# Optimization experiments

Hardware: AMD Instinct MI355X
Metric: run time of the kernel (lower is better)

The kernel has to match this reference:

```python
import jax, jax.numpy as jnp
import numpy as np

B, DIM, N = 4, 256, 2048
DIM_CTX, M = 256, 2048
HEADS, DIM_HEAD = 8, 64
DIM_INNER = HEADS * DIM_HEAD  # 512
EPS = 1e-12  # matches F.normalize eps


def setup_inputs() -> dict:
    key = jax.random.key(0)
    ks = jax.random.split(key, 8)
    return {
        "fmap": jax.random.normal(ks[0], (B, DIM, N), dtype=jnp.float32),
        "context": jax.random.normal(ks[1], (B, DIM_CTX, M), dtype=jnp.float32),
        "mask": jax.random.randint(ks[2], (B, M), 0, 2) > 0,
        "gamma": jnp.ones((DIM, 1), dtype=jnp.float32),
        "gamma_ctx": jnp.ones((DIM_CTX, 1), dtype=jnp.float32),
        "Wq": jax.random.normal(ks[3], (DIM_INNER, DIM), dtype=jnp.float32) * (DIM ** -0.5),
        "Wkv": jax.random.normal(ks[4], (2 * DIM_INNER, DIM_CTX), dtype=jnp.float32) * (DIM_CTX ** -0.5),
        "Wout": jax.random.normal(ks[5], (DIM, DIM_INNER), dtype=jnp.float32) * (DIM_INNER ** -0.5),
    }


def channel_rmsnorm(x, gamma):
    # F.normalize(x, dim=1) * sqrt(dim) * gamma ; x: [b, c, n], gamma: [c, 1]
    scale = x.shape[1] ** 0.5
    norm = jnp.sqrt(jnp.sum(x * x, axis=1, keepdims=True))
    normed = x / jnp.maximum(norm, EPS)
    return normed * scale * gamma[None]


def reference(fmap, context, mask, gamma, gamma_ctx, Wq, Wkv, Wout):
    h, d = HEADS, DIM_HEAD
    attn_scale = d ** -0.5

    fmap_n = channel_rmsnorm(fmap, gamma)          # [b, dim, n]
    ctx_n = channel_rmsnorm(context, gamma_ctx)    # [b, dim_ctx, m]

    # 1x1 Conv1d == matmul over channels
    q = jnp.einsum('oc,bcn->bon', Wq, fmap_n)      # [b, h*d, n]
    kv = jnp.einsum('oc,bcm->bom', Wkv, ctx_n)     # [b, 2*h*d, m]
    k, v = jnp.split(kv, 2, axis=1)

    # [b, h*d, n] -> [b, h, n, d]
    def to_heads(t):
        b, _, nn = t.shape
        return t.reshape(b, h, d, nn).transpose(0, 1, 3, 2)

    q, k, v = to_heads(q), to_heads(k), to_heads(v)

    # L2-distance attention: sim = -||q_i - k_j||_2 * scale
    q2 = jnp.sum(q * q, axis=-1)                   # [b, h, n]
    k2 = jnp.sum(k * k, axis=-1)                   # [b, h, m]
    qk = jnp.einsum('bhid,bhjd->bhij', q, k)       # [b, h, n, m]
    d2 = jnp.maximum(q2[..., :, None] + k2[..., None, :] - 2.0 * qk, 0.0)
    dist = jnp.sqrt(jnp.maximum(d2, EPS))
    sim = -dist * attn_scale

    neg_max = -jnp.finfo(sim.dtype).max
    sim = jnp.where(mask[:, None, None, :], sim, neg_max)

    attn = jax.nn.softmax(sim, axis=-1)            # [b, h, n, m]
    out = jnp.einsum('bhij,bhjd->bhid', attn, v)   # [b, h, n, d]
    out = out.transpose(0, 1, 3, 2).reshape(out.shape[0], h * d, -1)  # [b, h*d, n]
    return jnp.einsum('oc,bcn->bon', Wout, out)    # [b, dim, n]
```

## Files before the change

### kernel.cpp

```cpp
#include <hip/hip_runtime.h>
#include <hip/hip_bf16.h>

#define B_ 4
#define DIM_ 256
#define N_ 2048
#define M_ 2048
#define HEADS_ 8
#define DHEAD_ 64
#define DINNER_ 512

typedef __attribute__((ext_vector_type(8))) short short8;
typedef __attribute__((ext_vector_type(4))) short short4v;
typedef __attribute__((ext_vector_type(4))) float floatx4;
typedef __attribute__((ext_vector_type(4))) _Float16 half4;
typedef __attribute__((ext_vector_type(8))) _Float16 half8;

#if defined(__has_builtin)
#if __has_builtin(__builtin_amdgcn_global_load_lds)
#define HAS_DMA 1
#endif
#endif

typedef __attribute__((address_space(1))) const void gvoid_t;
typedef __attribute__((address_space(3))) void lvoid_t;

__device__ inline short bf16r(float x) {
  unsigned u = __float_as_uint(x);
  unsigned r = (u + 0x7fffu + ((u >> 16) & 1u)) >> 16;
  return (short)r;
}
__device__ inline float bf2f(short b) {
  return __uint_as_float(((unsigned)(unsigned short)b) << 16);
}

__global__ __launch_bounds__(256) void wsplit_kernel(
    const float* __restrict__ Wq, const float* __restrict__ Wkv,
    const float* __restrict__ Wout, const float* __restrict__ gamma,
    const float* __restrict__ gctx, short* __restrict__ whi,
    short* __restrict__ wlo) {
  const int y = blockIdx.y;
  const int gsz[3] = {32768, 65536, 32768};
  const int goff[3] = {0, 131072, 393216};
  int gidx = blockIdx.x * 256 + threadIdx.x;
  if (gidx >= gsz[y]) return;
  const float* W = (y == 0) ? Wq : (y == 1) ? Wkv : Wout;
  const int cmask = (y == 2) ? 511 : 255;
  int e0 = gidx * 4;
  int c = e0 & cmask;
  float4 wv = *(const float4*)&W[e0];
  if (y < 2) {
    const float* g = (y == 0) ? gamma : gctx;
    float4 g4 = *(const float4*)&g[c];
    wv.x *= g4.x; wv.y *= g4.y; wv.z *= g4.z; wv.w *= g4.w;
  }
  float vv[4] = {wv.x, wv.y, wv.z, wv.w};
  short4v hi, lo;
#pragma unroll
  for (int e = 0; e < 4; ++e) {
    short hb = bf16r(vv[e]);
    hi[e] = hb;
    lo[e] = bf16r(vv[e] - bf2f(hb));
  }
  *(short4v*)&whi[goff[y] + e0] = hi;
  *(short4v*)&wlo[goff[y] + e0] = lo;
}

__global__ __launch_bounds__(256) void colnorm_t_kernel(
    const float* __restrict__ xf, const float* __restrict__ xc,
    short* __restrict__ xtf, short* __restrict__ xtc, int NN) {
  const float* x = (blockIdx.z == 0) ? xf : xc;
  short* xt = (blockIdx.z == 0) ? xtf : xtc;
  int b = blockIdx.y;
  int tx = threadIdx.x, ty = threadIdx.y;
  int n0 = blockIdx.x * 64, n = n0 + tx;
  const float* xb = x + (size_t)b * 256 * NN;

  float ssq = 0.f;
  for (int c = ty; c < 256; c += 4) {
    float v = xb[(size_t)c * NN + n];
    ssq += v * v;
  }
  __shared__ float red[4][64];
  __shared__ float scl[64];
  __shared__ float t[64][65];
  red[ty][tx] = ssq;
  __syncthreads();
  if (ty == 0) {
    float s = red[0][tx] + red[1][tx] + red[2][tx] + red[3][tx];
    scl[tx] = 16.0f / fmaxf(sqrtf(s), 1e-12f);
  }
  int tid = ty * 64 + tx;
  int row = tid >> 2, cg = tid & 3;
  for (int c0 = 0; c0 < 256; c0 += 64) {
    __syncthreads();
    for (int cc = ty; cc < 64; cc += 4) t[cc][tx] = xb[(size_t)(c0 + cc) * NN + n];
    __syncthreads();
    float sc = scl[row];
    short8 o0v, o1v;
#pragma unroll
    for (int e = 0; e < 8; ++e) {
      o0v[e] = bf16r(t[cg * 16 + e][row] * sc);
      o1v[e] = bf16r(t[cg * 16 + 8 + e][row] * sc);
    }
    size_t base = ((size_t)b * NN + n0 + row) * 256 + c0 + cg * 16;
    *(short8*)&xt[base] = o0v;
    *(short8*)&xt[base + 8] = o1v;
  }
}

__global__ __launch_bounds__(256) void qkv_gemm_kernel(
    const short* __restrict__ whi, const short* __restrict__ wlo,
    const short* __restrict__ fmap_t, const short* __restrict__ ctx_t,
    short* __restrict__ qb, short* __restrict__ kc, _Float16* __restrict__ vc,
    const int* __restrict__ maskp, float* __restrict__ k2m) {
  const int b = blockIdx.z;
  const int y = blockIdx.y;
  const bool isq = (y < 4);
  const int o0 = (isq ? y : y - 4) * 128;
  const int n0 = blockIdx.x * 128;
  const short* Wh = whi + (isq ? 0 : 131072);
  const short* Wl = wlo + (isq ? 0 : 131072);
  const short* Xt = isq ? fmap_t : ctx_t;

  const int tid = threadIdx.x;
  const int w = tid >> 6, l = tid & 63, quad = l >> 4, l15 = l & 15;
  const int wo = (w >> 1) * 64, wn = (w & 1) * 64;

  __shared__ __align__(16) short Wa[2][128][40];
  __shared__ __align__(16) short Xb[128][40];

  floatx4 acc[4][4];
#pragma unroll
  for (int ot = 0; ot < 4; ++ot)
#pragma unroll
    for (int nt = 0; nt < 4; ++nt)
#pragma unroll
      for (int r = 0; r < 4; ++r) acc[ot][nt][r] = 0.f;

  for (int c0 = 0; c0 < 256; c0 += 32) {
    __syncthreads();
#pragma unroll
    for (int it = 0; it < 2; ++it) {
      int lin = tid + it * 256;
      int row = lin >> 2, sg = (lin & 3) * 8;
      size_t src = (size_t)(o0 + row) * 256 + c0 + sg;
      *(short8*)&Wa[0][row][sg] = *(const short8*)&Wh[src];
      *(short8*)&Wa[1][row][sg] = *(const short8*)&Wl[src];
    }
#pragma unroll
    for (int it = 0; it < 2; ++it) {
      int lin = tid + it * 256;
      int nn = lin >> 2, sg = (lin & 3) * 8;
      *(short8*)&Xb[nn][sg] =
          *(const short8*)&Xt[((size_t)b * 2048 + n0 + nn) * 256 + c0 + sg];
    }
    __syncthreads();

    short8 ah[4], al[4], bx[4];
#pragma unroll
    for (int ot = 0; ot < 4; ++ot) {
      ah[ot] = *(const short8*)&Wa[0][wo + 16 * ot + l15][8 * quad];
      al[ot] = *(const short8*)&Wa[1][wo + 16 * ot + l15][8 * quad];
    }
#pragma unroll
    for (int nt = 0; nt < 4; ++nt)
      bx[nt] = *(const short8*)&Xb[wn + 16 * nt + l15][8 * quad];
#pragma unroll
    for (int ot = 0; ot < 4; ++ot)
#pragma unroll
      for (int nt = 0; nt < 4; ++nt) {
        acc[ot][nt] =
            __builtin_amdgcn_mfma_f32_16x16x32_bf16(al[ot], bx[nt], acc[ot][nt], 0, 0, 0);
        acc[ot][nt] =
            __builtin_amdgcn_mfma_f32_16x16x32_bf16(ah[ot], bx[nt], acc[ot][nt], 0, 0, 0);
      }
  }

  if (isq) {
#pragma unroll
    for (int nt = 0; nt < 4; ++nt) {
      int n = n0 + wn + 16 * nt + l15;
      size_t base = ((size_t)b * 2048 + n) * 512;
#pragma unroll
      for (int ot = 0; ot < 4; ++ot) {
        int o = o0 + wo + 16 * ot + 4 * quad;
        short4v pk;
#pragma unroll
        for (int r = 0; r < 4; ++r) pk[r] = bf16r(acc[ot][nt][r]);
        *(short4v*)&qb[base + o] = pk;
      }
    }
  } else if (o0 < 512) {
    const int head = (o0 + wo) >> 6;
    const int bh = b * 8 + head;
    float k2p[4] = {0.f, 0.f, 0.f, 0.f};
#pragma unroll
    for (int nt = 0; nt < 4; ++nt) {
      int m = n0 + wn + 16 * nt + l15;
      int chunk = m >> 6, mrow = m & 63;
      size_t tbase = (((size_t)bh * 32 + chunk) * 64 + mrow) * 64;
      int sw = mrow & 7;
#pragma unroll
      for (int ot = 0; ot < 4; ++ot) {
        int d0 = 16 * ot + 4 * quad;
        short4v pk;
#pragma unroll
        for (int r = 0; r < 4; ++r) {
          short pv = bf16r(-2.0f * acc[ot][nt][r]);
          pk[r] = pv;
          float kr = bf2f(pv);
          k2p[nt] += kr * kr;
        }
        *(short4v*)&kc[tbase + (size_t)(((d0 >> 3) ^ sw) << 3) + (d0 & 7)] = pk;
      }
    }
#pragma unroll
    for (int nt = 0; nt < 4; ++nt) {
      float s = k2p[nt];
      s += __shfl_xor(s, 16);
      s += __shfl_xor(s, 32);
      if (quad == 0) {
        int m = n0 + wn + 16 * nt + l15;
        int mv = maskp[b * 2048 + m];
        k2m[(size_t)bh * 2048 + m] = mv ? 0.25f * s : __builtin_inff();
      }
    }
  } else {
    const int chv = o0 - 512 + wo;
    const int bh = b * 8 + (chv >> 6);
#pragma unroll
    for (int nt = 0; nt < 4; ++nt) {
      int j = n0 + wn + 16 * nt + l15;
      int chunk = j >> 6, jr = j & 63;
      int jrem = jr & 31;
      int colp = 32 * (jr >> 5) + ((jrem >> 2) & 3) * 8 + (jrem >> 4) * 4 +
                 (jrem & 3);
      size_t cbase = ((size_t)bh * 32 + chunk) * 4096;
#pragma unroll
      for (int ot = 0; ot < 4; ++ot)
#pragma unroll
        for (int r = 0; r < 4; ++r) {
          int drow = (chv + 16 * ot + 4 * quad + r) & 63;
          vc[cbase + drow * 64 + (((colp >> 3) ^ (drow & 7)) << 3) +
             (colp & 7)] = (_Float16)acc[ot][nt][r];
        }
    }
  }
}

__global__ __launch_bounds__(256, 4) void attn_kernel(
    const short* __restrict__ qb, const short* __restrict__ kc,
    const _Float16* __restrict__ vc, const float* __restrict__ k2m,
    short* __restrict__ attn_t) {
  const int bid = blockIdx.x;
  const int rr = bid & 7, qq = bid >> 3;
  const int bh = rr * 4 + (qq >> 5);
  const int iblk = qq & 31;
  const int h = bh & 7, b = bh >> 3;
  const int i0 = iblk * 64;

  const int tid = threadIdx.x;
  const int w = tid >> 6, l = tid & 63, quad = l >> 4, l15 = l & 15;

  __shared__ __align__(16) short kbuf[2][4096];
  __shared__ __align__(16) short vbuf[2][4096];

  const short* qrow =
      qb + ((size_t)b * 2048 + i0 + 16 * w + l15) * 512 + h * 64;
  const short* kcb = kc + (size_t)bh * 32 * 4096;
  const _Float16* vcb = vc + (size_t)bh * 32 * 4096;
  const float* k2b = k2m + (size_t)bh * 2048;

  short8 qa0 = *(const short8*)&qrow[8 * quad];
  short8 qa1 = *(const short8*)&qrow[32 + 8 * quad];
  float q2p = 0.f;
#pragma unroll
  for (int jj = 0; jj < 8; ++jj) {
    float f0 = bf2f(qa0[jj]), f1 = bf2f(qa1[jj]);
    q2p += f0 * f0 + f1 * f1;
  }
  q2p += __shfl_xor(q2p, 16);
  q2p += __shfl_xor(q2p, 32);
  const float q2c = q2p;

  floatx4 accO[4];
#pragma unroll
  for (int dt = 0; dt < 4; ++dt)
#pragma unroll
    for (int r = 0; r < 4; ++r) accO[dt][r] = 0.f;
  float lsum = 0.f;

  const float C2 = -0.18033688011112042f;
  const int sx = l15 & 7;

  auto stage = [&](int c, int p) {
    const short* ks = kcb + (size_t)c * 4096 + (2 * w) * 512 + l * 8;
    const _Float16* vs = vcb + (size_t)c * 4096 + (2 * w) * 512 + l * 8;
#ifdef HAS_DMA
    __builtin_amdgcn_global_load_lds((gvoid_t*)ks,
                                     (lvoid_t*)&kbuf[p][(2 * w) * 512], 16, 0, 0);
    __builtin_amdgcn_global_load_lds((gvoid_t*)(ks + 512),
                                     (lvoid_t*)&kbuf[p][(2 * w + 1) * 512], 16, 0, 0);
    __builtin_amdgcn_global_load_lds((gvoid_t*)vs,
                                     (lvoid_t*)&vbuf[p][(2 * w) * 512], 16, 0, 0);
    __builtin_amdgcn_global_load_lds((gvoid_t*)(vs + 512),
                                     (lvoid_t*)&vbuf[p][(2 * w + 1) * 512], 16, 0, 0);
#else
    *(short8*)&kbuf[p][(2 * w) * 512 + l * 8] = *(const short8*)ks;
    *(short8*)&kbuf[p][(2 * w + 1) * 512 + l * 8] = *(const short8*)(ks + 512);
    *(half8*)&vbuf[p][(2 * w) * 512 + l * 8] = *(const half8*)vs;
    *(half8*)&vbuf[p][(2 * w + 1) * 512 + l * 8] = *(const half8*)(vs + 512);
#endif
  };

  float4 k2pref[4];
#pragma unroll
  for (int jt = 0; jt < 4; ++jt)
    k2pref[jt] = *(const float4*)&k2b[16 * jt + 4 * quad];

  stage(0, 0);
  for (int c = 0; c < 32; ++c) {
    __syncthreads();
    if (c < 31) stage(c + 1, (c + 1) & 1);
    const int p = c & 1;

    float4 k2cur[4];
#pragma unroll
    for (int jt = 0; jt < 4; ++jt) k2cur[jt] = k2pref[jt];
    if (c < 31) {
#pragma unroll
      for (int jt = 0; jt < 4; ++jt)
        k2pref[jt] = *(const float4*)&k2b[(c + 1) * 64 + 16 * jt + 4 * quad];
    }

    half4 pb[4];
#pragma unroll
    for (int jt = 0; jt < 4; ++jt) {
      const short* kr = &kbuf[p][(16 * jt + l15) * 64];
      short8 k0 = *(const short8*)&kr[(quad ^ sx) << 3];
      short8 k1 = *(const short8*)&kr[((quad + 4) ^ sx) << 3];
      floatx4 a;
      a[0] = q2c; a[1] = q2c; a[2] = q2c; a[3] = q2c;
      a = __builtin_amdgcn_mfma_f32_16x16x32_bf16(k0, qa0, a, 0, 0, 0);
      a = __builtin_amdgcn_mfma_f32_16x16x32_bf16(k1, qa1, a, 0, 0, 0);
      float k2a[4] = {k2cur[jt].x, k2cur[jt].y, k2cur[jt].z, k2cur[jt].w};
#pragma unroll
      for (int r = 0; r < 4; ++r) {
        float d2 = fmaxf(a[r] + k2a[r], 1e-12f);
        float pv = __builtin_amdgcn_exp2f(C2 * __builtin_amdgcn_sqrtf(d2));
        lsum += pv;
        pb[jt][r] = (_Float16)pv;
      }
    }

#pragma unroll
    for (int dt = 0; dt < 4; ++dt) {
      const _Float16* vr = (const _Float16*)&vbuf[p][(16 * dt + l15) * 64];
      half8 h0 = *(const half8*)&vr[(quad ^ sx) << 3];
      half8 h1 = *(const half8*)&vr[((quad + 4) ^ sx) << 3];
      half4 va00 = __builtin_shufflevector(h0, h0, 0, 1, 2, 3);
      half4 va01 = __builtin_shufflevector(h0, h0, 4, 5, 6, 7);
      half4 va10 = __builtin_shufflevector(h1, h1, 0, 1, 2, 3);
      half4 va11 = __builtin_shufflevector(h1, h1, 4, 5, 6, 7);
      accO[dt] = __builtin_amdgcn_mfma_f32_16x16x16f16(va00, pb[0], accO[dt], 0, 0, 0);
      accO[dt] = __builtin_amdgcn_mfma_f32_16x16x16f16(va01, pb[1], accO[dt], 0, 0, 0);
      accO[dt] = __builtin_amdgcn_mfma_f32_16x16x16f16(va10, pb[2], accO[dt], 0, 0, 0);
      accO[dt] = __builtin_amdgcn_mfma_f32_16x16x16f16(va11, pb[3], accO[dt], 0, 0, 0);
    }
  }

  lsum += __shfl_xor(lsum, 16);
  lsum += __shfl_xor(lsum, 32);
  float rl = 1.0f / lsum;
  size_t base = ((size_t)b * 2048 + i0 + 16 * w + l15) * 512 + h * 64;
#pragma unroll
  for (int dt = 0; dt < 4; ++dt)
#pragma unroll
    for (int r = 0; r < 4; ++r)
      attn_t[base + 16 * dt + 4 * quad + r] = bf16r(accO[dt][r] * rl);
}

__global__ __launch_bounds__(256) void outproj_kernel(
    const short* __restrict__ whi, const short* __restrict__ wlo,
    const short* __restrict__ Xt, float* __restrict__ Yf) {
  const int b = blockIdx.z;
  const int n0 = blockIdx.x * 128;
  const int o0 = blockIdx.y * 64;
  const int tid = threadIdx.x;
  const int w = tid >> 6, l = tid & 63, quad = l >> 4, l15 = l & 15;
  const int wo = (w >> 1) * 32, wn = (w & 1) * 64;

  __shared__ __align__(16) short Wa[2][64][40];
  __shared__ __align__(16) short Xb[128][40];

  floatx4 acc[2][4];
#pragma unroll
  for (int ot = 0; ot < 2; ++ot)
#pragma unroll
    for (int nt = 0; nt < 4; ++nt)
#pragma unroll
      for (int r = 0; r < 4; ++r) acc[ot][nt][r] = 0.f;

  for (int c0 = 0; c0 < 512; c0 += 32) {
    __syncthreads();
    {
      int row = tid >> 2, sg = (tid & 3) * 8;
      size_t src = (size_t)(o0 + row) * 512 + c0 + sg;
      *(short8*)&Wa[0][row][sg] = *(const short8*)&whi[src];
      *(short8*)&Wa[1][row][sg] = *(const short8*)&wlo[src];
    }
#pragma unroll
    for (int it = 0; it < 2; ++it) {
      int lin = tid + it * 256;
      int nn = lin >> 2, sg = (lin & 3) * 8;
      *(short8*)&Xb[nn][sg] =
          *(const short8*)&Xt[((size_t)b * 2048 + n0 + nn) * 512 + c0 + sg];
    }
    __syncthreads();

    short8 ah[2], al[2], bx[4];
#pragma unroll
    for (int ot = 0; ot < 2; ++ot) {
      ah[ot] = *(const short8*)&Wa[0][wo + 16 * ot + l15][8 * quad];
      al[ot] = *(const short8*)&Wa[1][wo + 16 * ot + l15][8 * quad];
    }
#pragma unroll
    for (int nt = 0; nt < 4; ++nt)
      bx[nt] = *(const short8*)&Xb[wn + 16 * nt + l15][8 * quad];
#pragma unroll
    for (int ot = 0; ot < 2; ++ot)
#pragma unroll
      for (int nt = 0; nt < 4; ++nt) {
        acc[ot][nt] =
            __builtin_amdgcn_mfma_f32_16x16x32_bf16(al[ot], bx[nt], acc[ot][nt], 0, 0, 0);
        acc[ot][nt] =
            __builtin_amdgcn_mfma_f32_16x16x32_bf16(ah[ot], bx[nt], acc[ot][nt], 0, 0, 0);
      }
  }

#pragma unroll
  for (int ot = 0; ot < 2; ++ot)
#pragma unroll
    for (int r = 0; r < 4; ++r) {
      int o = o0 + wo + 16 * ot + 4 * quad + r;
#pragma unroll
      for (int nt = 0; nt < 4; ++nt)
        Yf[((size_t)b * 256 + o) * 2048 + n0 + wn + 16 * nt + l15] =
            acc[ot][nt][r];
    }
}

extern "C" void kernel_launch(void* const* d_in, const int* in_sizes, int n_in,
                              void* d_out, int out_size, void* d_ws,
                              size_t ws_size, hipStream_t stream) {
  const float* fmap = (const float*)d_in[0];
  const float* context = (const float*)d_in[1];
  const int* mask = (const int*)d_in[2];
  const float* gamma = (const float*)d_in[3];
  const float* gamma_ctx = (const float*)d_in[4];
  const float* Wq = (const float*)d_in[5];
  const float* Wkv = (const float*)d_in[6];
  const float* Wout = (const float*)d_in[7];
  float* out = (float*)d_out;

  char* ws = (char*)d_ws;
  short* fmap_t = (short*)ws;
  short* ctx_t = fmap_t + 2097152;
  short* qb = ctx_t + 2097152;
  short* kc = qb + 4194304;
  _Float16* vc = (_Float16*)(kc + 4194304);
  short* attn_t = (short*)(vc + 4194304);
  float* k2m = (float*)(attn_t + 4194304);
  short* whi = (short*)(k2m + 65536);
  short* wlo = whi + 524288;

  dim3 blk64x4(64, 4);
  wsplit_kernel<<<dim3(256, 3), 256, 0, stream>>>(Wq, Wkv, Wout, gamma,
                                                  gamma_ctx, whi, wlo);
  colnorm_t_kernel<<<dim3(32, B_, 2), blk64x4, 0, stream>>>(
      fmap, context, fmap_t, ctx_t, N_);
  qkv_gemm_kernel<<<dim3(16, 12, B_), 256, 0, stream>>>(
      whi, wlo, fmap_t, ctx_t, qb, kc, vc, mask, k2m);
  attn_kernel<<<dim3(1024), 256, 0, stream>>>(qb, kc, vc, k2m, attn_t);
  outproj_kernel<<<dim3(16, 4, B_), 256, 0, stream>>>(whi + 393216,
                                                      wlo + 393216, attn_t,
                                                      out);
}
```

Before: 215.7 us.

## Split attention key chunks across wave pairs and fold softmax scale into Q/K

Result: faster. 209.6 us (-2.8%).

```diff
diff --git a/kernel.cpp b/kernel.cpp
--- a/kernel.cpp
+++ b/kernel.cpp
@@ -23,6 +23,10 @@
 
 typedef __attribute__((address_space(1))) const void gvoid_t;
 typedef __attribute__((address_space(3))) void lvoid_t;
+
+#define CQ_ 0.18033688011112042f
+#define NEG2CQ_ (-0.36067376022224084f)
+#define EPS2_ 3.25213893e-14f
 
 __device__ inline short bf16r(float x) {
   unsigned u = __float_as_uint(x);
@@ -186,7 +190,7 @@
         int o = o0 + wo + 16 * ot + 4 * quad;
         short4v pk;
 #pragma unroll
-        for (int r = 0; r < 4; ++r) pk[r] = bf16r(acc[ot][nt][r]);
+        for (int r = 0; r < 4; ++r) pk[r] = bf16r(CQ_ * acc[ot][nt][r]);
         *(short4v*)&qb[base + o] = pk;
       }
     }
@@ -206,7 +210,7 @@
         short4v pk;
 #pragma unroll
         for (int r = 0; r < 4; ++r) {
-          short pv = bf16r(-2.0f * acc[ot][nt][r]);
+          short pv = bf16r(NEG2CQ_ * acc[ot][nt][r]);
           pk[r] = pv;
           float kr = bf2f(pv);
           k2p[nt] += kr * kr;
@@ -248,7 +252,7 @@
   }
 }
 
-__global__ __launch_bounds__(256, 4) void attn_kernel(
+__global__ __launch_bounds__(512, 8) void attn_kernel(
     const short* __restrict__ qb, const short* __restrict__ kc,
     const _Float16* __restrict__ vc, const float* __restrict__ k2m,
     short* __restrict__ attn_t) {
@@ -261,12 +265,12 @@
 
   const int tid = threadIdx.x;
   const int w = tid >> 6, l = tid & 63, quad = l >> 4, l15 = l & 15;
-
-  __shared__ __align__(16) short kbuf[2][4096];
-  __shared__ __align__(16) short vbuf[2][4096];
+  const int wr = w >> 1, jh = w & 1;
+
+  __shared__ __align__(16) short sbuf[2][2][4096];
 
   const short* qrow =
-      qb + ((size_t)b * 2048 + i0 + 16 * w + l15) * 512 + h * 64;
+      qb + ((size_t)b * 2048 + i0 + 16 * wr + l15) * 512 + h * 64;
   const short* kcb = kc + (size_t)bh * 32 * 4096;
   const _Float16* vcb = vc + (size_t)bh * 32 * 4096;
   const float* k2b = k2m + (size_t)bh * 2048;
@@ -290,94 +294,97 @@
     for (int r = 0; r < 4; ++r) accO[dt][r] = 0.f;
   float lsum = 0.f;
 
-  const float C2 = -0.18033688011112042f;
   const int sx = l15 & 7;
 
   auto stage = [&](int c, int p) {
-    const short* ks = kcb + (size_t)c * 4096 + (2 * w) * 512 + l * 8;
-    const _Float16* vs = vcb + (size_t)c * 4096 + (2 * w) * 512 + l * 8;
+    const short* ks = kcb + (size_t)c * 4096 + w * 512 + l * 8;
+    const _Float16* vs = vcb + (size_t)c * 4096 + w * 512 + l * 8;
 #ifdef HAS_DMA
     __builtin_amdgcn_global_load_lds((gvoid_t*)ks,
-                                     (lvoid_t*)&kbuf[p][(2 * w) * 512], 16, 0, 0);
-    __builtin_amdgcn_global_load_lds((gvoid_t*)(ks + 512),
-                                     (lvoid_t*)&kbuf[p][(2 * w + 1) * 512], 16, 0, 0);
+                                     (lvoid_t*)&sbuf[0][p][w * 512], 16, 0, 0);
     __builtin_amdgcn_global_load_lds((gvoid_t*)vs,
-                                     (lvoid_t*)&vbuf[p][(2 * w) * 512], 16, 0, 0);
-    __builtin_amdgcn_global_load_lds((gvoid_t*)(vs + 512),
-                                     (lvoid_t*)&vbuf[p][(2 * w + 1) * 512], 16, 0, 0);
+                                     (lvoid_t*)&sbuf[1][p][w * 512], 16, 0, 0);
 #else
-    *(short8*)&kbuf[p][(2 * w) * 512 + l * 8] = *(const short8*)ks;
-    *(short8*)&kbuf[p][(2 * w + 1) * 512 + l * 8] = *(const short8*)(ks + 512);
-    *(half8*)&vbuf[p][(2 * w) * 512 + l * 8] = *(const half8*)vs;
-    *(half8*)&vbuf[p][(2 * w + 1) * 512 + l * 8] = *(const half8*)(vs + 512);
+    *(short8*)&sbuf[0][p][w * 512 + l * 8] = *(const short8*)ks;
+    *(half8*)&((_Float16*)sbuf[1][p])[w * 512 + l * 8] = *(const half8*)vs;
 #endif
   };
 
-  float4 k2pref[4];
-#pragma unroll
-  for (int jt = 0; jt < 4; ++jt)
-    k2pref[jt] = *(const float4*)&k2b[16 * jt + 4 * quad];
-
   stage(0, 0);
   for (int c = 0; c < 32; ++c) {
     __syncthreads();
     if (c < 31) stage(c + 1, (c + 1) & 1);
     const int p = c & 1;
 
-    float4 k2cur[4];
-#pragma unroll
-    for (int jt = 0; jt < 4; ++jt) k2cur[jt] = k2pref[jt];
-    if (c < 31) {
-#pragma unroll
-      for (int jt = 0; jt < 4; ++jt)
-        k2pref[jt] = *(const float4*)&k2b[(c + 1) * 64 + 16 * jt + 4 * quad];
-    }
-
-    half4 pb[4];
-#pragma unroll
-    for (int jt = 0; jt < 4; ++jt) {
-      const short* kr = &kbuf[p][(16 * jt + l15) * 64];
+    half4 pb0, pb1;
+#pragma unroll
+    for (int jt = 0; jt < 2; ++jt) {
+      float4 k2v = *(const float4*)&k2b[c * 64 + jh * 32 + 16 * jt + 4 * quad];
+      const short* kr = &sbuf[0][p][(jh * 32 + 16 * jt + l15) * 64];
       short8 k0 = *(const short8*)&kr[(quad ^ sx) << 3];
       short8 k1 = *(const short8*)&kr[((quad + 4) ^ sx) << 3];
       floatx4 a;
-      a[0] = q2c; a[1] = q2c; a[2] = q2c; a[3] = q2c;
+      a[0] = q2c + k2v.x;
+      a[1] = q2c + k2v.y;
+      a[2] = q2c + k2v.z;
+      a[3] = q2c + k2v.w;
+      __builtin_amdgcn_s_setprio(1);
       a = __builtin_amdgcn_mfma_f32_16x16x32_bf16(k0, qa0, a, 0, 0, 0);
       a = __builtin_amdgcn_mfma_f32_16x16x32_bf16(k1, qa1, a, 0, 0, 0);
-      float k2a[4] = {k2cur[jt].x, k2cur[jt].y, k2cur[jt].z, k2cur[jt].w};
+      __builtin_amdgcn_s_setprio(0);
+      half4 pbt;
 #pragma unroll
       for (int r = 0; r < 4; ++r) {
-        float d2 = fmaxf(a[r] + k2a[r], 1e-12f);
-        float pv = __builtin_amdgcn_exp2f(C2 * __builtin_amdgcn_sqrtf(d2));
+        float s = __builtin_amdgcn_sqrtf(fmaxf(a[r], EPS2_));
+        float pv = __builtin_amdgcn_exp2f(-s);
         lsum += pv;
-        pb[jt][r] = (_Float16)pv;
-      }
-    }
-
+        pbt[r] = (_Float16)pv;
+      }
+      if (jt == 0) pb0 = pbt; else pb1 = pbt;
+    }
+
+    __builtin_amdgcn_s_setprio(1);
 #pragma unroll
     for (int dt = 0; dt < 4; ++dt) {
-      const _Float16* vr = (const _Float16*)&vbuf[p][(16 * dt + l15) * 64];
-      half8 h0 = *(const half8*)&vr[(quad ^ sx) << 3];
-      half8 h1 = *(const half8*)&vr[((quad + 4) ^ sx) << 3];
-      half4 va00 = __builtin_shufflevector(h0, h0, 0, 1, 2, 3);
-      half4 va01 = __builtin_shufflevector(h0, h0, 4, 5, 6, 7);
-      half4 va10 = __builtin_shufflevector(h1, h1, 0, 1, 2, 3);
-      half4 va11 = __builtin_shufflevector(h1, h1, 4, 5, 6, 7);
-      accO[dt] = __builtin_amdgcn_mfma_f32_16x16x16f16(va00, pb[0], accO[dt], 0, 0, 0);
-      accO[dt] = __builtin_amdgcn_mfma_f32_16x16x16f16(va01, pb[1], accO[dt], 0, 0, 0);
-      accO[dt] = __builtin_amdgcn_mfma_f32_16x16x16f16(va10, pb[2], accO[dt], 0, 0, 0);
-      accO[dt] = __builtin_amdgcn_mfma_f32_16x16x16f16(va11, pb[3], accO[dt], 0, 0, 0);
-    }
-  }
-
-  lsum += __shfl_xor(lsum, 16);
-  lsum += __shfl_xor(lsum, 32);
-  float rl = 1.0f / lsum;
-  size_t base = ((size_t)b * 2048 + i0 + 16 * w + l15) * 512 + h * 64;
-#pragma unroll
-  for (int dt = 0; dt < 4; ++dt)
-#pragma unroll
-    for (int r = 0; r < 4; ++r)
-      attn_t[base + 16 * dt + 4 * quad + r] = bf16r(accO[dt][r] * rl);
+      const _Float16* vr = (const _Float16*)&sbuf[1][p][(16 * dt + l15) * 64];
+      half8 hh = *(const half8*)&vr[((quad + 4 * jh) ^ sx) << 3];
+      half4 vaA = __builtin_shufflevector(hh, hh, 0, 1, 2, 3);
+      half4 vaB = __builtin_shufflevector(hh, hh, 4, 5, 6, 7);
+      accO[dt] = __builtin_amdgcn_mfma_f32_16x16x16f16(vaA, pb0, accO[dt], 0, 0, 0);
+      accO[dt] = __builtin_amdgcn_mfma_f32_16x16x16f16(vaB, pb1, accO[dt], 0, 0, 0);
+    }
+    __builtin_amdgcn_s_setprio(0);
+  }
+
+  __syncthreads();
+  float* scr = (float*)sbuf;
+  const int sidx = (wr * 64 + l) * 17;
+  if (jh) {
+#pragma unroll
+    for (int dt = 0; dt < 4; ++dt)
+#pragma unroll
+      for (int r = 0; r < 4; ++r) scr[sidx + dt * 4 + r] = accO[dt][r];
+    scr[sidx + 16] = lsum;
+  }
+  __syncthreads();
+  if (!jh) {
+#pragma unroll
+    for (int dt = 0; dt < 4; ++dt)
+#pragma unroll
+      for (int r = 0; r < 4; ++r) accO[dt][r] += scr[sidx + dt * 4 + r];
+    lsum += scr[sidx + 16];
+    lsum += __shfl_xor(lsum, 16);
+    lsum += __shfl_xor(lsum, 32);
+    float rl = 1.0f / lsum;
+    size_t base = ((size_t)b * 2048 + i0 + 16 * wr + l15) * 512 + h * 64;
+#pragma unroll
+    for (int dt = 0; dt < 4; ++dt) {
+      short4v pk;
+#pragma unroll
+      for (int r = 0; r < 4; ++r) pk[r] = bf16r(accO[dt][r] * rl);
+      *(short4v*)&attn_t[base + 16 * dt + 4 * quad] = pk;
+    }
+  }
 }
 
 __global__ __launch_bounds__(256) void outproj_kernel(
@@ -481,7 +488,7 @@
       fmap, context, fmap_t, ctx_t, N_);
   qkv_gemm_kernel<<<dim3(16, 12, B_), 256, 0, stream>>>(
       whi, wlo, fmap_t, ctx_t, qb, kc, vc, mask, k2m);
-  attn_kernel<<<dim3(1024), 256, 0, stream>>>(qb, kc, vc, k2m, attn_t);
+  attn_kernel<<<dim3(1024), 512, 0, stream>>>(qb, kc, vc, k2m, attn_t);
   outproj_kernel<<<dim3(16, 4, B_), 256, 0, stream>>>(whi + 393216,
                                                       wlo + 393216, attn_t,
                                                       out);
```
